# Optimization experiments

Measured on AMD Instinct MI355X. Metric: run time of the kernel, lower is better.

## Reference

```python
import jax, jax.numpy as jnp
import numpy as np

B, H, S, Dh = 2, 16, 2048, 64
SPARSITY = 0.1

def _make_pattern(key, seq_len, sparsity):
    # Faithful to torch: randperm over S*S, take first num_connections, set diagonal True
    num_connections = int(seq_len * seq_len * sparsity)
    perm = jax.random.permutation(key, seq_len * seq_len)
    idx = perm[:num_connections]
    rows = idx // seq_len
    cols = idx % seq_len
    pat = jnp.zeros((seq_len, seq_len), dtype=bool).at[rows, cols].set(True)
    diag = jnp.arange(seq_len)
    return pat.at[diag, diag].set(True)

def setup_inputs() -> dict:
    key = jax.random.key(0)
    kq, kk, kv, kp = jax.random.split(key, 4)
    return {
        "query": jax.random.normal(kq, (B, H, S, Dh), dtype=jnp.float32),
        "key": jax.random.normal(kk, (B, H, S, Dh), dtype=jnp.float32),
        "value": jax.random.normal(kv, (B, H, S, Dh), dtype=jnp.float32),
        "pattern": _make_pattern(kp, S, SPARSITY),  # [S,S] bool
    }

def reference(query, key, value, pattern):
    head_dim = query.shape[-1]
    scale = 1.0 / np.sqrt(head_dim).astype(np.float32)
    # [B,H,S,S] dense scores
    scores = jnp.einsum("bhqd,bhkd->bhqk", query, key) * scale
    # masked_fill(~pattern, -1e9); pattern broadcasts over B,H
    scores = jnp.where(pattern[None, None, :, :], scores, jnp.float32(-1e9))
    attn = jax.nn.softmax(scores, axis=-1)
    return jnp.einsum("bhqk,bhkd->bhqd", attn, value)
```

## Files before the change

### kernel.cpp

```cpp
#include <hip/hip_runtime.h>
#include <hip/hip_bf16.h>

#define S_LEN 2048
#define DH 64
#define BH_N 32

typedef __attribute__((ext_vector_type(8))) short bf16x8;
typedef __attribute__((ext_vector_type(4))) float f32x4;
typedef __attribute__((ext_vector_type(16))) float f32x16;
typedef __attribute__((ext_vector_type(2))) unsigned int u32x2;
typedef __attribute__((ext_vector_type(4))) unsigned int u32x4;
typedef unsigned long long u64;
typedef unsigned int u32;

static constexpr size_t OFF_PM   = 0;
static constexpr size_t OFF_COMB = 524288;
static constexpr size_t WS_NEED  = OFF_COMB + 16777216;

__device__ __forceinline__ unsigned short f2bf(float f) {
  unsigned int u = __float_as_uint(f);
  u += 0x7fffu + ((u >> 16) & 1u);
  return (unsigned short)(u >> 16);
}

__device__ __forceinline__ u32 cvt_pk_bf16(float lo, float hi_) {
  u32 r;
  asm("v_cvt_pk_bf16_f32 %0, %1, %2" : "=v"(r) : "v"(lo), "v"(hi_));
  return r;
}

__device__ __forceinline__ f32x16 zero16() {
  f32x16 z;
#pragma unroll
  for (int i = 0; i < 16; ++i) z[i] = 0.f;
  return z;
}

__device__ __forceinline__ void glds16(const short* g, short* l) {
  __builtin_amdgcn_global_load_lds((const __attribute__((address_space(1))) unsigned int*)(g),
                                   (__attribute__((address_space(3))) unsigned int*)(l),
                                   16, 0, 0);
}

__global__ __launch_bounds__(256) void prep_kernel(
    const float* __restrict__ K, const float* __restrict__ V,
    const void* __restrict__ pat, short* __restrict__ Comb, u64* __restrict__ pmw) {
  __shared__ short tlds[DH][72];
  const int tid = threadIdx.x;
  const int b = blockIdx.x;
  if (b < 2048) {
    const int flat = b * 256 + tid;
    const int s = flat & 7, r = (flat >> 3) & 63, t = (flat >> 9) & 31, bh = flat >> 14;
    const float* kp = K + (((size_t)bh * S_LEN + t * 64 + r) * DH + s * 8);
    float ka[8];
    *(float4*)&ka[0] = *(const float4*)&kp[0];
    *(float4*)&ka[4] = *(const float4*)&kp[4];
    short ks[8];
#pragma unroll
    for (int j = 0; j < 8; ++j) ks[j] = (short)f2bf(ka[j]);
    short* dst = Comb + ((size_t)bh * 32 + t) * 8192 + r * 64 + ((s ^ (r & 7)) * 8);
    *(bf16x8*)dst = *(const bf16x8*)&ks[0];
  } else if (b < 3072) {
    const int bb = b - 2048;
    const int bh = bb >> 5, t = bb & 31;
    const int row = tid >> 2, cg = (tid & 3) * 16;
    const float* vp = V + (((size_t)bh * S_LEN + t * 64 + row) * DH + cg);
    float vf[16];
#pragma unroll
    for (int j = 0; j < 16; j += 4) *(float4*)&vf[j] = *(const float4*)&vp[j];
#pragma unroll
    for (int j = 0; j < 16; ++j) tlds[cg + j][row] = (short)f2bf(vf[j]);
    __syncthreads();
    short* vbase = Comb + ((size_t)bh * 32 + t) * 8192 + 4096;
#pragma unroll
    for (int i = 0; i < 2; ++i) {
      const int ch = tid + i * 256;
      const int r = ch >> 3, s = ch & 7;
      *(bf16x8*)&vbase[r * 64 + s * 8] = *(const bf16x8*)&tlds[r][(s ^ (r & 7)) * 8];
    }
  } else {
    const int wdi = (b - 3072) * 256 + tid;
    const int row = wdi >> 5, t = wdi & 31;
    const unsigned char* p8 = (const unsigned char*)pat;
    const bool isU8 = (p8[(size_t)row * (S_LEN + 1)] == 1) &&
                      (p8[(size_t)(row ^ 1) * (S_LEN + 1)] == 1);
    u64 bits = 0;
    if (isU8) {
      const u64* p = (const u64*)pat + (size_t)row * 256 + t * 8;
#pragma unroll
      for (int q = 0; q < 8; ++q) {
        u64 x = p[q] & 0x0101010101010101ull;
        bits |= ((x * 0x0102040810204080ull) >> 56) << (q * 8);
      }
    } else {
      const int* p = (const int*)pat + (size_t)row * S_LEN + t * 64;
#pragma unroll 8
      for (int j = 0; j < 64; ++j)
        bits |= (u64)(p[j] != 0) << j;
    }
    pmw[wdi] = bits;
  }
}

__global__ __launch_bounds__(512, 4) void sattn7_kernel(
    const float* __restrict__ Qf, const short* __restrict__ Comb,
    const u64* __restrict__ pm, float* __restrict__ out) {
  __shared__ short buf[2][2][8192];

  const int tid  = threadIdx.x;
  const int w    = tid >> 6;
  const int half = w >> 2;
  const int wq   = w & 3;
  const int lane = tid & 63;
  const int ql   = lane & 31;
  const int hi   = lane >> 5;
  const int ht   = tid & 255;

  const int lin  = blockIdx.y * 16 + blockIdx.x;
  const int nlin = (lin & 7) * 64 + (lin >> 3);
  const int bx   = nlin & 15;
  const int bh   = nlin >> 4;

  const int q = bx * 128 + wq * 32 + ql;
  const size_t base = (size_t)bh * (S_LEN * DH);

  const short* src = Comb + ((size_t)bh * 32 + half * 16) * 8192;
  const u64* pmrow = pm + (size_t)q * 32 + half * 16;

  const float sc = 0.18033688f;
  bf16x8 qf[4];
  {
    const float* qp = Qf + base + (size_t)q * DH;
#pragma unroll
    for (int t = 0; t < 4; ++t) {
      float v[8];
      *(float4*)&v[0] = *(const float4*)&qp[t * 16 + hi * 8];
      *(float4*)&v[4] = *(const float4*)&qp[t * 16 + hi * 8 + 4];
#pragma unroll
      for (int j = 0; j < 8; ++j) qf[t][j] = (short)f2bf(v[j] * sc);
    }
  }

  int rdo[4];
#pragma unroll
  for (int f = 0; f < 4; ++f)
    rdo[f] = ql * 64 + (((2 * f + hi) ^ ql) & 7) * 8;

#pragma unroll
  for (int i = 0; i < 4; ++i)
    glds16(src + i * 2048 + ht * 8, &buf[half][0][i * 2048 + ht * 8]);
  u64 wd = pmrow[0], wdn = pmrow[1];
  __syncthreads();

  f32x16 accO0 = zero16(), accO1 = zero16(), accL = zero16();
  bf16x8 ones;
#pragma unroll
  for (int j = 0; j < 8; ++j) ones[j] = (short)0x3F80;

#pragma unroll 2
  for (int t = 0; t < 16; ++t) {
    const int cur = t & 1;
    const short* ktc = buf[half][cur];
    const short* vtc = ktc + 4096;
    if (t < 15) {
      const short* gs = src + (size_t)(t + 1) * 8192;
#pragma unroll
      for (int i = 0; i < 4; ++i)
        glds16(gs + i * 2048 + ht * 8, &buf[half][cur ^ 1][i * 2048 + ht * 8]);
    }

    const u32 wlo = (u32)(wd >> (hi * 4));
    const u32 whi = (u32)(wd >> (hi * 4 + 32));
    wd = wdn;
    if (t + 2 < 16) wdn = pmrow[t + 2];

#pragma unroll
    for (int h = 0; h < 2; ++h) {
      const int ro = h * 2048;
      const u32 wm = h ? whi : wlo;
      f32x16 a = zero16();
      __builtin_amdgcn_s_setprio(1);
#pragma unroll
      for (int f = 0; f < 4; ++f) {
        bf16x8 kv = *(const bf16x8*)&ktc[rdo[f] + ro];
        a = __builtin_amdgcn_mfma_f32_32x32x16_bf16(kv, qf[f], a, 0, 0, 0);
      }
      __builtin_amdgcn_s_setprio(0);
      float p[16];
#pragma unroll
      for (int j = 0; j < 16; ++j) {
        const int pos = (j & 3) + 8 * (j >> 2);
        p[j] = __uint_as_float(__float_as_uint(__builtin_amdgcn_exp2f(a[j])) &
                               (u32)__builtin_amdgcn_sbfe(wm, pos, 1));
      }
      __builtin_amdgcn_s_setprio(1);
#pragma unroll
      for (int f2 = 0; f2 < 2; ++f2) {
        const int o = f2 * 8;
        const u32 A = cvt_pk_bf16(p[o + 0], p[o + 1]);
        const u32 B = cvt_pk_bf16(p[o + 2], p[o + 3]);
        const u32 C = cvt_pk_bf16(p[o + 4], p[o + 5]);
        const u32 D = cvt_pk_bf16(p[o + 6], p[o + 7]);
        const u32x2 r02 = __builtin_amdgcn_permlane32_swap(A, C, false, false);
        const u32x2 r13 = __builtin_amdgcn_permlane32_swap(B, D, false, false);
        u32x4 fw = {r02[0], r13[0], r02[1], r13[1]};
        const bf16x8 pbv = __builtin_bit_cast(bf16x8, fw);
        const int fv = h * 2 + f2;
        bf16x8 av0 = *(const bf16x8*)&vtc[rdo[fv]];
        accO0 = __builtin_amdgcn_mfma_f32_32x32x16_bf16(av0, pbv, accO0, 0, 0, 0);
        bf16x8 av1 = *(const bf16x8*)&vtc[rdo[fv] + 2048];
        accO1 = __builtin_amdgcn_mfma_f32_32x32x16_bf16(av1, pbv, accO1, 0, 0, 0);
        accL = __builtin_amdgcn_mfma_f32_32x32x16_bf16(ones, pbv, accL, 0, 0, 0);
      }
      __builtin_amdgcn_s_setprio(0);
    }
    __syncthreads();
  }

  float* xo = (float*)buf;
  const int xbase = (wq * 64 + lane) * 33;
  if (half == 1) {
#pragma unroll
    for (int j = 0; j < 16; ++j) xo[xbase + j] = accO0[j];
#pragma unroll
    for (int j = 0; j < 16; ++j) xo[xbase + 16 + j] = accO1[j];
    xo[8448 + wq * 64 + lane] = accL[0];
  }
  __syncthreads();
  if (half == 0) {
    const float l1 = xo[8448 + wq * 64 + lane];
    const float rl = 1.f / (accL[0] + l1);
#pragma unroll
    for (int j = 0; j < 16; ++j) accO0[j] = (accO0[j] + xo[xbase + j]) * rl;
#pragma unroll
    for (int j = 0; j < 16; ++j) accO1[j] = (accO1[j] + xo[xbase + 16 + j]) * rl;
    float* op = out + base + (size_t)q * DH;
#pragma unroll
    for (int g = 0; g < 4; ++g) {
      f32x4 o0 = {accO0[4 * g + 0], accO0[4 * g + 1], accO0[4 * g + 2], accO0[4 * g + 3]};
      *(f32x4*)&op[8 * g + 4 * hi] = o0;
      f32x4 o1 = {accO1[4 * g + 0], accO1[4 * g + 1], accO1[4 * g + 2], accO1[4 * g + 3]};
      *(f32x4*)&op[32 + 8 * g + 4 * hi] = o1;
    }
  }
}

__global__ __launch_bounds__(256) void detect_pat_kernel(const unsigned char* __restrict__ p,
                                                         int* __restrict__ flag) {
  const int i = blockIdx.x * 256 + threadIdx.x;
  const int cnt = (p[(size_t)i * (S_LEN + 1)] == 1) ? 1 : 0;
  atomicAdd(flag, cnt);
}

__global__ __launch_bounds__(256) void sattn_fb_kernel(
    const float* __restrict__ Q, const float* __restrict__ K,
    const float* __restrict__ V, const void* __restrict__ pat,
    float* __restrict__ out, const int* __restrict__ flag) {
  __shared__ short kt[64][72];
  __shared__ short vt[DH][72];
  __shared__ short pb[4][16][72];
  const int tid = threadIdx.x;
  const int w = tid >> 6, lane = tid & 63, g = lane >> 4, c = lane & 15;
  const int bh = blockIdx.y, q0 = blockIdx.x * 64;
  const size_t base = (size_t)bh * S_LEN * DH;
  const bool isU8 = (*flag == S_LEN);
  const unsigned char* __restrict__ p8 = (const unsigned char*)pat;
  const int* __restrict__ p32 = (const int*)pat;
  bf16x8 aQ[2];
  {
    const int qr = q0 + w * 16 + c;
    const float* qp = Q + base + (size_t)qr * DH + g * 8;
#pragma unroll
    for (int ch = 0; ch < 2; ++ch)
#pragma unroll
      for (int j = 0; j < 8; ++j) aQ[ch][j] = (short)f2bf(qp[ch * 32 + j]);
  }
  f32x4 accO[4];
#pragma unroll
  for (int n = 0; n < 4; ++n) accO[n] = (f32x4){0.f, 0.f, 0.f, 0.f};
  float m[4], l[4];
#pragma unroll
  for (int r = 0; r < 4; ++r) { m[r] = -1e30f; l[r] = 0.f; }
  const int qs = q0 + w * 16 + g * 4;
  for (int k0 = 0; k0 < S_LEN; k0 += 64) {
    __syncthreads();
    {
      const int row = tid >> 2, cg = (tid & 3) * 16;
      const float* kp = K + base + (size_t)(k0 + row) * DH + cg;
      const float* vp = V + base + (size_t)(k0 + row) * DH + cg;
      float kf[16], vf[16];
#pragma unroll
      for (int j = 0; j < 16; j += 4) {
        *(float4*)&kf[j] = *(const float4*)&kp[j];
        *(float4*)&vf[j] = *(const float4*)&vp[j];
      }
      short ks[16];
#pragma unroll
      for (int j = 0; j < 16; ++j) ks[j] = (short)f2bf(kf[j]);
      *(bf16x8*)&kt[row][cg] = *(const bf16x8*)&ks[0];
      *(bf16x8*)&kt[row][cg + 8] = *(const bf16x8*)&ks[8];
#pragma unroll
      for (int j = 0; j < 16; ++j) vt[cg + j][row] = (short)f2bf(vf[j]);
    }
    __syncthreads();
    f32x4 sf[4];
#pragma unroll
    for (int n = 0; n < 4; ++n) {
      f32x4 acc = (f32x4){0.f, 0.f, 0.f, 0.f};
#pragma unroll
      for (int ch = 0; ch < 2; ++ch) {
        bf16x8 bk = *(const bf16x8*)&kt[n * 16 + c][ch * 32 + g * 8];
        acc = __builtin_amdgcn_mfma_f32_16x16x32_bf16(aQ[ch], bk, acc, 0, 0, 0);
      }
      sf[n] = acc;
    }
    float sv[4][4];
#pragma unroll
    for (int r = 0; r < 4; ++r) {
      if (isU8) {
        const unsigned char* prow = p8 + (size_t)(qs + r) * S_LEN + k0 + c;
#pragma unroll
        for (int n = 0; n < 4; ++n) sv[n][r] = prow[n * 16] ? sf[n][r] * 0.125f : -1e30f;
      } else {
        const int* prow = p32 + (size_t)(qs + r) * S_LEN + k0 + c;
#pragma unroll
        for (int n = 0; n < 4; ++n) sv[n][r] = prow[n * 16] ? sf[n][r] * 0.125f : -1e30f;
      }
    }
#pragma unroll
    for (int r = 0; r < 4; ++r) {
      float tm = fmaxf(fmaxf(sv[0][r], sv[1][r]), fmaxf(sv[2][r], sv[3][r]));
      tm = fmaxf(tm, __shfl_xor(tm, 1));
      tm = fmaxf(tm, __shfl_xor(tm, 2));
      tm = fmaxf(tm, __shfl_xor(tm, 4));
      tm = fmaxf(tm, __shfl_xor(tm, 8));
      const float mn = fmaxf(m[r], tm);
      const float alpha = __expf(m[r] - mn);
      m[r] = mn;
      float rs = 0.f, pr[4];
#pragma unroll
      for (int n = 0; n < 4; ++n) {
        const float p = (sv[n][r] > -1e29f) ? __expf(sv[n][r] - mn) : 0.f;
        pr[n] = p; rs += p;
      }
      rs += __shfl_xor(rs, 1);
      rs += __shfl_xor(rs, 2);
      rs += __shfl_xor(rs, 4);
      rs += __shfl_xor(rs, 8);
      l[r] = l[r] * alpha + rs;
#pragma unroll
      for (int n = 0; n < 4; ++n) {
        accO[n][r] *= alpha;
        pb[w][g * 4 + r][n * 16 + c] = (short)f2bf(pr[n]);
      }
    }
    bf16x8 pa[2];
#pragma unroll
    for (int ch = 0; ch < 2; ++ch) pa[ch] = *(const bf16x8*)&pb[w][c][ch * 32 + g * 8];
#pragma unroll
    for (int n = 0; n < 4; ++n)
#pragma unroll
      for (int ch = 0; ch < 2; ++ch) {
        bf16x8 vb = *(const bf16x8*)&vt[n * 16 + c][ch * 32 + g * 8];
        accO[n] = __builtin_amdgcn_mfma_f32_16x16x32_bf16(pa[ch], vb, accO[n], 0, 0, 0);
      }
  }
  float rl[4];
#pragma unroll
  for (int r = 0; r < 4; ++r) rl[r] = 1.f / l[r];
  float* op = out + base;
#pragma unroll
  for (int n = 0; n < 4; ++n)
#pragma unroll
    for (int r = 0; r < 4; ++r)
      op[(size_t)(qs + r) * DH + n * 16 + c] = accO[n][r] * rl[r];
}

extern "C" void kernel_launch(void* const* d_in, const int* in_sizes, int n_in,
                              void* d_out, int out_size, void* d_ws, size_t ws_size,
                              hipStream_t stream) {
  const float* Q = (const float*)d_in[0];
  const float* K = (const float*)d_in[1];
  const float* V = (const float*)d_in[2];
  const void* pat = d_in[3];
  float* out = (float*)d_out;
  char* ws = (char*)d_ws;

  if (ws_size >= WS_NEED) {
    u64*   pmw  = (u64*)(ws + OFF_PM);
    short* Comb = (short*)(ws + OFF_COMB);
    prep_kernel<<<3328, 256, 0, stream>>>(K, V, pat, Comb, pmw);
    sattn7_kernel<<<dim3(16, BH_N), 512, 0, stream>>>(Q, Comb, pmw, out);
  } else {
    int* flag = (int*)ws;
    hipMemsetAsync(flag, 0, sizeof(int), stream);
    detect_pat_kernel<<<8, 256, 0, stream>>>((const unsigned char*)pat, flag);
    sattn_fb_kernel<<<dim3(S_LEN / 64, BH_N), 256, 0, stream>>>(Q, K, V, pat, out, flag);
  }
}
```

Measured before the change: 71.11 us.

## Compute softmax denominator with VALU adds instead of ones-MFMA; transpose mask layout

Drops the third MFMA per PV step that multiplied a ones matrix by P to get the row sum. Instead each lane sums its 16 masked exp values in registers and combines lane halves with permlane32_swap at the end. The packed mask words are stored tile-major (t*2048+row) so neighbouring query lanes read contiguous words, and the LDS buffer is flattened with explicit offsets. This cuts MFMA work by about a quarter in the PV stage at the cost of extra VALU adds. Summing in fp32 rather than on bf16-rounded P values slightly changes numerics.

```diff
diff --git a/kernel.cpp b/kernel.cpp
--- a/kernel.cpp
+++ b/kernel.cpp
@@ -27,6 +27,11 @@
   u32 r;
   asm("v_cvt_pk_bf16_f32 %0, %1, %2" : "=v"(r) : "v"(lo), "v"(hi_));
   return r;
+}
+
+__device__ __forceinline__ float pair_sum(float x) {
+  u32x2 r = __builtin_amdgcn_permlane32_swap(__float_as_uint(x), __float_as_uint(x), false, false);
+  return __uint_as_float(r[0]) + __uint_as_float(r[1]);
 }
 
 __device__ __forceinline__ f32x16 zero16() {
@@ -79,8 +84,9 @@
       *(bf16x8*)&vbase[r * 64 + s * 8] = *(const bf16x8*)&tlds[r][(s ^ (r & 7)) * 8];
     }
   } else {
-    const int wdi = (b - 3072) * 256 + tid;
-    const int row = wdi >> 5, t = wdi & 31;
+    const int bb = b - 3072;
+    const int t = bb >> 3, rg = bb & 7;
+    const int row = rg * 256 + tid;
     const unsigned char* p8 = (const unsigned char*)pat;
     const bool isU8 = (p8[(size_t)row * (S_LEN + 1)] == 1) &&
                       (p8[(size_t)(row ^ 1) * (S_LEN + 1)] == 1);
@@ -98,14 +104,14 @@
       for (int j = 0; j < 64; ++j)
         bits |= (u64)(p[j] != 0) << j;
     }
-    pmw[wdi] = bits;
-  }
-}
-
-__global__ __launch_bounds__(512, 4) void sattn7_kernel(
+    pmw[(size_t)t * 2048 + row] = bits;
+  }
+}
+
+__global__ __launch_bounds__(512, 4) void sattn8_kernel(
     const float* __restrict__ Qf, const short* __restrict__ Comb,
     const u64* __restrict__ pm, float* __restrict__ out) {
-  __shared__ short buf[2][2][8192];
+  __shared__ short buf[32768];
 
   const int tid  = threadIdx.x;
   const int w    = tid >> 6;
@@ -125,7 +131,7 @@
   const size_t base = (size_t)bh * (S_LEN * DH);
 
   const short* src = Comb + ((size_t)bh * 32 + half * 16) * 8192;
-  const u64* pmrow = pm + (size_t)q * 32 + half * 16;
+  const u64* pml = pm + (size_t)(half * 16) * 2048 + q;
 
   const float sc = 0.18033688f;
   bf16x8 qf[4];
@@ -144,45 +150,44 @@
   int rdo[4];
 #pragma unroll
   for (int f = 0; f < 4; ++f)
-    rdo[f] = ql * 64 + (((2 * f + hi) ^ ql) & 7) * 8;
+    rdo[f] = half * 16384 + ql * 64 + (((2 * f + hi) ^ ql) & 7) * 8;
+  const int hb = half * 16384 + ht * 8;
 
 #pragma unroll
   for (int i = 0; i < 4; ++i)
-    glds16(src + i * 2048 + ht * 8, &buf[half][0][i * 2048 + ht * 8]);
-  u64 wd = pmrow[0], wdn = pmrow[1];
+    glds16(src + i * 2048 + ht * 8, &buf[hb + i * 2048]);
+  u64 wd = pml[0], wdn = pml[2048];
   __syncthreads();
 
-  f32x16 accO0 = zero16(), accO1 = zero16(), accL = zero16();
-  bf16x8 ones;
-#pragma unroll
-  for (int j = 0; j < 8; ++j) ones[j] = (short)0x3F80;
+  f32x16 accO0 = zero16(), accO1 = zero16();
+  const f32x16 Z = zero16();
+  float lloc = 0.f;
 
 #pragma unroll 2
   for (int t = 0; t < 16; ++t) {
     const int cur = t & 1;
-    const short* ktc = buf[half][cur];
-    const short* vtc = ktc + 4096;
     if (t < 15) {
       const short* gs = src + (size_t)(t + 1) * 8192;
 #pragma unroll
       for (int i = 0; i < 4; ++i)
-        glds16(gs + i * 2048 + ht * 8, &buf[half][cur ^ 1][i * 2048 + ht * 8]);
+        glds16(gs + i * 2048 + ht * 8, &buf[hb + (cur ^ 1) * 8192 + i * 2048]);
     }
 
     const u32 wlo = (u32)(wd >> (hi * 4));
     const u32 whi = (u32)(wd >> (hi * 4 + 32));
     wd = wdn;
-    if (t + 2 < 16) wdn = pmrow[t + 2];
+    if (t + 2 < 16) wdn = pml[(t + 2) * 2048];
 
 #pragma unroll
     for (int h = 0; h < 2; ++h) {
-      const int ro = h * 2048;
+      const int ro = cur * 8192 + h * 2048;
       const u32 wm = h ? whi : wlo;
-      f32x16 a = zero16();
       __builtin_amdgcn_s_setprio(1);
-#pragma unroll
-      for (int f = 0; f < 4; ++f) {
-        bf16x8 kv = *(const bf16x8*)&ktc[rdo[f] + ro];
+      f32x16 a = __builtin_amdgcn_mfma_f32_32x32x16_bf16(
+          *(const bf16x8*)&buf[rdo[0] + ro], qf[0], Z, 0, 0, 0);
+#pragma unroll
+      for (int f = 1; f < 4; ++f) {
+        bf16x8 kv = *(const bf16x8*)&buf[rdo[f] + ro];
         a = __builtin_amdgcn_mfma_f32_32x32x16_bf16(kv, qf[f], a, 0, 0, 0);
       }
       __builtin_amdgcn_s_setprio(0);
@@ -192,6 +197,13 @@
         const int pos = (j & 3) + 8 * (j >> 2);
         p[j] = __uint_as_float(__float_as_uint(__builtin_amdgcn_exp2f(a[j])) &
                                (u32)__builtin_amdgcn_sbfe(wm, pos, 1));
+      }
+      {
+        float s0 = (p[0] + p[1]) + (p[2] + p[3]);
+        float s1 = (p[4] + p[5]) + (p[6] + p[7]);
+        float s2 = (p[8] + p[9]) + (p[10] + p[11]);
+        float s3 = (p[12] + p[13]) + (p[14] + p[15]);
+        lloc += (s0 + s1) + (s2 + s3);
       }
       __builtin_amdgcn_s_setprio(1);
 #pragma unroll
@@ -206,16 +218,17 @@
         u32x4 fw = {r02[0], r13[0], r02[1], r13[1]};
         const bf16x8 pbv = __builtin_bit_cast(bf16x8, fw);
         const int fv = h * 2 + f2;
-        bf16x8 av0 = *(const bf16x8*)&vtc[rdo[fv]];
+        bf16x8 av0 = *(const bf16x8*)&buf[rdo[fv] + cur * 8192 + 4096];
         accO0 = __builtin_amdgcn_mfma_f32_32x32x16_bf16(av0, pbv, accO0, 0, 0, 0);
-        bf16x8 av1 = *(const bf16x8*)&vtc[rdo[fv] + 2048];
+        bf16x8 av1 = *(const bf16x8*)&buf[rdo[fv] + cur * 8192 + 4096 + 2048];
         accO1 = __builtin_amdgcn_mfma_f32_32x32x16_bf16(av1, pbv, accO1, 0, 0, 0);
-        accL = __builtin_amdgcn_mfma_f32_32x32x16_bf16(ones, pbv, accL, 0, 0, 0);
       }
       __builtin_amdgcn_s_setprio(0);
     }
     __syncthreads();
   }
+
+  const float lfull = pair_sum(lloc);
 
   float* xo = (float*)buf;
   const int xbase = (wq * 64 + lane) * 33;
@@ -224,12 +237,12 @@
     for (int j = 0; j < 16; ++j) xo[xbase + j] = accO0[j];
 #pragma unroll
     for (int j = 0; j < 16; ++j) xo[xbase + 16 + j] = accO1[j];
-    xo[8448 + wq * 64 + lane] = accL[0];
+    xo[8448 + wq * 64 + lane] = lfull;
   }
   __syncthreads();
   if (half == 0) {
     const float l1 = xo[8448 + wq * 64 + lane];
-    const float rl = 1.f / (accL[0] + l1);
+    const float rl = 1.f / (lfull + l1);
 #pragma unroll
     for (int j = 0; j < 16; ++j) accO0[j] = (accO0[j] + xo[xbase + j]) * rl;
 #pragma unroll
@@ -390,7 +403,7 @@
     u64*   pmw  = (u64*)(ws + OFF_PM);
     short* Comb = (short*)(ws + OFF_COMB);
     prep_kernel<<<3328, 256, 0, stream>>>(K, V, pat, Comb, pmw);
-    sattn7_kernel<<<dim3(16, BH_N), 512, 0, stream>>>(Q, Comb, pmw, out);
+    sattn8_kernel<<<dim3(16, BH_N), 512, 0, stream>>>(Q, Comb, pmw, out);
   } else {
     int* flag = (int*)ws;
     hipMemsetAsync(flag, 0, sizeof(int), stream);
```

Result: slower. 77.15 us (+8.5%).

## Transpose pattern bitmask layout and interleave two QK MFMA chains per tile

Applied to the files above, without the earlier changes.

The prep kernel now stores the packed mask words tile-major ([tile][row]) rather than row-major. Consecutive query lanes therefore read consecutive u64 words, so the per-iteration mask loads coalesce. The attention loop also computes both 32-key halves' QK^T MFMAs in one interleaved pass with two independent accumulators, then does the exp/mask and PV steps. This exposes more MFMA-level parallelism at the cost of extra registers, which may matter under the 512x4 launch bounds.

```diff
diff --git a/kernel.cpp b/kernel.cpp
--- a/kernel.cpp
+++ b/kernel.cpp
@@ -79,8 +79,9 @@
       *(bf16x8*)&vbase[r * 64 + s * 8] = *(const bf16x8*)&tlds[r][(s ^ (r & 7)) * 8];
     }
   } else {
-    const int wdi = (b - 3072) * 256 + tid;
-    const int row = wdi >> 5, t = wdi & 31;
+    const int bb = b - 3072;
+    const int t = bb >> 3, rg = bb & 7;
+    const int row = rg * 256 + tid;
     const unsigned char* p8 = (const unsigned char*)pat;
     const bool isU8 = (p8[(size_t)row * (S_LEN + 1)] == 1) &&
                       (p8[(size_t)(row ^ 1) * (S_LEN + 1)] == 1);
@@ -98,11 +99,11 @@
       for (int j = 0; j < 64; ++j)
         bits |= (u64)(p[j] != 0) << j;
     }
-    pmw[wdi] = bits;
-  }
-}
-
-__global__ __launch_bounds__(512, 4) void sattn7_kernel(
+    pmw[(size_t)t * 2048 + row] = bits;
+  }
+}
+
+__global__ __launch_bounds__(512, 4) void sattn9_kernel(
     const float* __restrict__ Qf, const short* __restrict__ Comb,
     const u64* __restrict__ pm, float* __restrict__ out) {
   __shared__ short buf[2][2][8192];
@@ -125,7 +126,7 @@
   const size_t base = (size_t)bh * (S_LEN * DH);
 
   const short* src = Comb + ((size_t)bh * 32 + half * 16) * 8192;
-  const u64* pmrow = pm + (size_t)q * 32 + half * 16;
+  const u64* pml = pm + (size_t)(half * 16) * 2048 + q;
 
   const float sc = 0.18033688f;
   bf16x8 qf[4];
@@ -149,7 +150,7 @@
 #pragma unroll
   for (int i = 0; i < 4; ++i)
     glds16(src + i * 2048 + ht * 8, &buf[half][0][i * 2048 + ht * 8]);
-  u64 wd = pmrow[0], wdn = pmrow[1];
+  u64 wd = pml[0], wdn = pml[2048];
   __syncthreads();
 
   f32x16 accO0 = zero16(), accO1 = zero16(), accL = zero16();
@@ -172,48 +173,49 @@
     const u32 wlo = (u32)(wd >> (hi * 4));
     const u32 whi = (u32)(wd >> (hi * 4 + 32));
     wd = wdn;
-    if (t + 2 < 16) wdn = pmrow[t + 2];
-
-#pragma unroll
-    for (int h = 0; h < 2; ++h) {
-      const int ro = h * 2048;
-      const u32 wm = h ? whi : wlo;
-      f32x16 a = zero16();
-      __builtin_amdgcn_s_setprio(1);
-#pragma unroll
-      for (int f = 0; f < 4; ++f) {
-        bf16x8 kv = *(const bf16x8*)&ktc[rdo[f] + ro];
-        a = __builtin_amdgcn_mfma_f32_32x32x16_bf16(kv, qf[f], a, 0, 0, 0);
-      }
-      __builtin_amdgcn_s_setprio(0);
-      float p[16];
-#pragma unroll
-      for (int j = 0; j < 16; ++j) {
-        const int pos = (j & 3) + 8 * (j >> 2);
-        p[j] = __uint_as_float(__float_as_uint(__builtin_amdgcn_exp2f(a[j])) &
-                               (u32)__builtin_amdgcn_sbfe(wm, pos, 1));
-      }
-      __builtin_amdgcn_s_setprio(1);
-#pragma unroll
-      for (int f2 = 0; f2 < 2; ++f2) {
-        const int o = f2 * 8;
-        const u32 A = cvt_pk_bf16(p[o + 0], p[o + 1]);
-        const u32 B = cvt_pk_bf16(p[o + 2], p[o + 3]);
-        const u32 C = cvt_pk_bf16(p[o + 4], p[o + 5]);
-        const u32 D = cvt_pk_bf16(p[o + 6], p[o + 7]);
-        const u32x2 r02 = __builtin_amdgcn_permlane32_swap(A, C, false, false);
-        const u32x2 r13 = __builtin_amdgcn_permlane32_swap(B, D, false, false);
-        u32x4 fw = {r02[0], r13[0], r02[1], r13[1]};
-        const bf16x8 pbv = __builtin_bit_cast(bf16x8, fw);
-        const int fv = h * 2 + f2;
-        bf16x8 av0 = *(const bf16x8*)&vtc[rdo[fv]];
-        accO0 = __builtin_amdgcn_mfma_f32_32x32x16_bf16(av0, pbv, accO0, 0, 0, 0);
-        bf16x8 av1 = *(const bf16x8*)&vtc[rdo[fv] + 2048];
-        accO1 = __builtin_amdgcn_mfma_f32_32x32x16_bf16(av1, pbv, accO1, 0, 0, 0);
-        accL = __builtin_amdgcn_mfma_f32_32x32x16_bf16(ones, pbv, accL, 0, 0, 0);
-      }
-      __builtin_amdgcn_s_setprio(0);
-    }
+    if (t + 2 < 16) wdn = pml[(t + 2) * 2048];
+
+    f32x16 a0 = zero16(), a1 = zero16();
+    __builtin_amdgcn_s_setprio(1);
+#pragma unroll
+    for (int f = 0; f < 4; ++f) {
+      bf16x8 k0v = *(const bf16x8*)&ktc[rdo[f]];
+      a0 = __builtin_amdgcn_mfma_f32_32x32x16_bf16(k0v, qf[f], a0, 0, 0, 0);
+      bf16x8 k1v = *(const bf16x8*)&ktc[rdo[f] + 2048];
+      a1 = __builtin_amdgcn_mfma_f32_32x32x16_bf16(k1v, qf[f], a1, 0, 0, 0);
+    }
+    __builtin_amdgcn_s_setprio(0);
+
+    float p0[16], p1[16];
+#pragma unroll
+    for (int j = 0; j < 16; ++j) {
+      const int pos = (j & 3) + 8 * (j >> 2);
+      p0[j] = __uint_as_float(__float_as_uint(__builtin_amdgcn_exp2f(a0[j])) &
+                              (u32)__builtin_amdgcn_sbfe(wlo, pos, 1));
+      p1[j] = __uint_as_float(__float_as_uint(__builtin_amdgcn_exp2f(a1[j])) &
+                              (u32)__builtin_amdgcn_sbfe(whi, pos, 1));
+    }
+
+    __builtin_amdgcn_s_setprio(1);
+#pragma unroll
+    for (int fv = 0; fv < 4; ++fv) {
+      const float* ps = (fv < 2) ? p0 : p1;
+      const int o = (fv & 1) * 8;
+      const u32 A = cvt_pk_bf16(ps[o + 0], ps[o + 1]);
+      const u32 B = cvt_pk_bf16(ps[o + 2], ps[o + 3]);
+      const u32 C = cvt_pk_bf16(ps[o + 4], ps[o + 5]);
+      const u32 D = cvt_pk_bf16(ps[o + 6], ps[o + 7]);
+      const u32x2 r02 = __builtin_amdgcn_permlane32_swap(A, C, false, false);
+      const u32x2 r13 = __builtin_amdgcn_permlane32_swap(B, D, false, false);
+      u32x4 fw = {r02[0], r13[0], r02[1], r13[1]};
+      const bf16x8 pbv = __builtin_bit_cast(bf16x8, fw);
+      bf16x8 av0 = *(const bf16x8*)&vtc[rdo[fv]];
+      accO0 = __builtin_amdgcn_mfma_f32_32x32x16_bf16(av0, pbv, accO0, 0, 0, 0);
+      bf16x8 av1 = *(const bf16x8*)&vtc[rdo[fv] + 2048];
+      accO1 = __builtin_amdgcn_mfma_f32_32x32x16_bf16(av1, pbv, accO1, 0, 0, 0);
+      accL = __builtin_amdgcn_mfma_f32_32x32x16_bf16(ones, pbv, accL, 0, 0, 0);
+    }
+    __builtin_amdgcn_s_setprio(0);
     __syncthreads();
   }
 
@@ -390,7 +392,7 @@
     u64*   pmw  = (u64*)(ws + OFF_PM);
     short* Comb = (short*)(ws + OFF_COMB);
     prep_kernel<<<3328, 256, 0, stream>>>(K, V, pat, Comb, pmw);
-    sattn7_kernel<<<dim3(16, BH_N), 512, 0, stream>>>(Q, Comb, pmw, out);
+    sattn9_kernel<<<dim3(16, BH_N), 512, 0, stream>>>(Q, Comb, pmw, out);
   } else {
     int* flag = (int*)ws;
     hipMemsetAsync(flag, 0, sizeof(int), stream);
```

Measured after the change: 69.24 us. 1.03x faster.
